# Optimization experiments

Measured on AMD Instinct MI355X. Metric: run time of the kernel, lower is better.

## Reference

```python
import jax, jax.numpy as jnp
import numpy as np

PLOGIT_INIT = 1.5

def setup_inputs() -> dict:
    key = jax.random.key(0)
    B, C, H, W = 32, 256, 64, 64
    x = jax.random.normal(key, (B, C, H, W), dtype=jnp.float32)
    plogit = jnp.full((C,), PLOGIT_INIT, dtype=jnp.float32)  # learned param (post channel-expansion)
    return {"input": x, "plogit": plogit}


def reference(input, plogit):
    B, C = input.shape[0], input.shape[1]
    x = input.reshape(B * C, -1)                       # [B*C, HW]  (to_cw)
    s = jnp.sort(x, axis=-1)                           # per-row full sort
    N = s.shape[1]
    p = jax.nn.sigmoid(plogit)                         # [C]
    # torch: p.view(1,-1).repeat(B,1).view(-1) -> channel-major tiling over batch
    p_full = jnp.tile(p, B)                            # [B*C]
    # torch indexes with int(N * p.data[0] -/+ 0.02): a single scalar column index
    p0 = jax.lax.stop_gradient(p[0])
    i_low = jnp.clip((N * (p0 - 0.02)).astype(jnp.int32), 0, N - 1)
    i_high = jnp.clip((N * (p0 + 0.02)).astype(jnp.int32), 0, N - 1)
    x_low = jax.lax.stop_gradient(jnp.take(s, i_low, axis=1))    # [B*C], detached
    x_high = jax.lax.stop_gradient(jnp.take(s, i_high, axis=1))  # [B*C], detached
    thr = x_low + (x_high - x_low) * p_full            # linear interp, grad flows via p
    thr = thr.reshape(B, C, 1, 1)                      # from_cw
    return jax.nn.relu(input - thr)
```

## Files before the change

kernel.cpp:

```cpp
#include <hip/hip_runtime.h>
#include <math.h>

#define NTHREADS 256
#define NELEM    4096
#define VPT      4
#define NPART    8
#define HSTRIDE  257

__device__ __forceinline__ unsigned f2ord(float f) {
    unsigned u = __float_as_uint(f);
    return (u & 0x80000000u) ? ~u : (u | 0x80000000u);
}
__device__ __forceinline__ float ord2f(unsigned k) {
    unsigned u = (k & 0x80000000u) ? (k ^ 0x80000000u) : ~k;
    return __uint_as_float(u);
}

__device__ __forceinline__ void histo_pass(const unsigned* keys, unsigned* hist,
                                           unsigned known, unsigned pref, int shift, int tid) {
    for (int i = tid; i < NPART * HSTRIDE; i += NTHREADS) hist[i] = 0u;
    __syncthreads();
    unsigned* myh = hist + (tid & (NPART - 1)) * HSTRIDE;
    const uint4* kp = (const uint4*)keys;
    #pragma unroll
    for (int j = 0; j < VPT; ++j) {
        uint4 kk = kp[j * NTHREADS + tid];
        unsigned karr[4] = {kk.x, kk.y, kk.z, kk.w};
        #pragma unroll
        for (int e = 0; e < 4; ++e) {
            unsigned k = karr[e];
            if ((k & known) == pref)
                atomicAdd(&myh[(k >> shift) & 0xFFu], 1u);
        }
    }
    __syncthreads();
}

__device__ __forceinline__ void scan_pick(const unsigned* hist, unsigned* scanbuf,
                                          int tid, unsigned rA, unsigned rB, bool doB,
                                          unsigned* sh) {
    unsigned cnt = 0;
    #pragma unroll
    for (int p = 0; p < NPART; ++p) cnt += hist[p * HSTRIDE + tid];
    scanbuf[tid] = cnt;
    __syncthreads();
    for (int off = 1; off < NTHREADS; off <<= 1) {
        unsigned add = (tid >= off) ? scanbuf[tid - off] : 0u;
        __syncthreads();
        scanbuf[tid] += add;
        __syncthreads();
    }
    unsigned inc = scanbuf[tid];
    unsigned exc = tid ? scanbuf[tid - 1] : 0u;
    if (rA >= exc && rA < inc) { sh[0] = (unsigned)tid; sh[1] = rA - exc; }
    if (doB && rB >= exc && rB < inc) { sh[2] = (unsigned)tid; sh[3] = rB - exc; }
    __syncthreads();
}

__global__ void __launch_bounds__(NTHREADS)
xsrelu_kernel(const float* __restrict__ x, const float* __restrict__ plogit,
              float* __restrict__ out, int C) {
    __shared__ __align__(16) unsigned keys[NELEM];
    __shared__ unsigned hist[NPART * HSTRIDE];
    __shared__ unsigned scanbuf[NTHREADS];
    __shared__ unsigned sh[4];

    const int tid = threadIdx.x;
    const int row = blockIdx.x;
    const float4* xr = (const float4*)(x + (size_t)row * NELEM);

    float4 v[VPT];
    #pragma unroll
    for (int j = 0; j < VPT; ++j) {
        v[j] = xr[j * NTHREADS + tid];
        int base = (j * NTHREADS + tid) * 4;
        keys[base + 0] = f2ord(v[j].x);
        keys[base + 1] = f2ord(v[j].y);
        keys[base + 2] = f2ord(v[j].z);
        keys[base + 3] = f2ord(v[j].w);
    }

    float p0 = 1.0f / (1.0f + expf(-plogit[0]));
    int c = row % C;
    float pc = 1.0f / (1.0f + expf(-plogit[c]));

    int kLow  = (int)((float)NELEM * (p0 - 0.02f));
    int kHigh = (int)((float)NELEM * (p0 + 0.02f));
    kLow  = min(max(kLow, 0),  NELEM - 1);
    kHigh = min(max(kHigh, 0), NELEM - 1);

    __syncthreads();

    unsigned prefA = 0, prefB = 0, known = 0;
    unsigned rA = (unsigned)kLow, rB = (unsigned)kHigh;
    bool diverged = false;

    for (int shift = 24; shift >= 0; shift -= 8) {
        histo_pass(keys, hist, known, prefA, shift, tid);
        scan_pick(hist, scanbuf, tid, rA, rB, !diverged, sh);
        unsigned bA = sh[0], nrA = sh[1];
        if (!diverged) {
            unsigned bB = sh[2], nrB = sh[3];
            prefB = prefA | (bB << shift);
            prefA = prefA | (bA << shift);
            rA = nrA; rB = nrB;
            if (bA != bB) diverged = true;
        } else {
            prefA |= (bA << shift);
            rA = nrA;
            histo_pass(keys, hist, known, prefB, shift, tid);
            scan_pick(hist, scanbuf, tid, rB, rB, false, sh);
            prefB |= (sh[0] << shift);
            rB = sh[1];
        }
        known |= (0xFFu << shift);
    }

    float xlow  = ord2f(prefA);
    float xhigh = ord2f(prefB);
    float thr = xlow + (xhigh - xlow) * pc;

    float4* outr = (float4*)(out + (size_t)row * NELEM);
    #pragma unroll
    for (int j = 0; j < VPT; ++j) {
        float4 o;
        o.x = fmaxf(v[j].x - thr, 0.0f);
        o.y = fmaxf(v[j].y - thr, 0.0f);
        o.z = fmaxf(v[j].z - thr, 0.0f);
        o.w = fmaxf(v[j].w - thr, 0.0f);
        outr[j * NTHREADS + tid] = o;
    }
}

extern "C" void kernel_launch(void* const* d_in, const int* in_sizes, int n_in,
                              void* d_out, int out_size, void* d_ws, size_t ws_size,
                              hipStream_t stream) {
    const float* x      = (const float*)d_in[0];
    const float* plogit = (const float*)d_in[1];
    float* out          = (float*)d_out;
    int C    = in_sizes[1];
    int rows = in_sizes[0] / NELEM;
    xsrelu_kernel<<<rows, NTHREADS, 0, stream>>>(x, plogit, out, C);
}
```

Measured before the change: 267.8 us.

## Replace shared-memory radix select with per-wave register bisection using ballot counts

Each wavefront now processes one row, holding its 4096 keys in registers (64 per lane), and finds the two order statistics by binary search over the 32-bit key space. Each step counts keys at or below the midpoint with ballot and popcount. This removes the shared-memory histograms, atomics, block-level scans and barriers. In exchange it performs up to 64 bisection steps of 64 compares each per row, and raises register pressure.

After: 366.9 us. 37.0% more time.

```diff
diff --git a/kernel.cpp b/kernel.cpp
--- a/kernel.cpp
+++ b/kernel.cpp
@@ -3,9 +3,7 @@
 
 #define NTHREADS 256
 #define NELEM    4096
-#define VPT      4
-#define NPART    8
-#define HSTRIDE  257
+#define EPL      64
 
 __device__ __forceinline__ unsigned f2ord(float f) {
     unsigned u = __float_as_uint(f);
@@ -16,68 +14,44 @@
     return __uint_as_float(u);
 }
 
-__device__ __forceinline__ void histo_pass(const unsigned* keys, unsigned* hist,
-                                           unsigned known, unsigned pref, int shift, int tid) {
-    for (int i = tid; i < NPART * HSTRIDE; i += NTHREADS) hist[i] = 0u;
-    __syncthreads();
-    unsigned* myh = hist + (tid & (NPART - 1)) * HSTRIDE;
-    const uint4* kp = (const uint4*)keys;
+__device__ __forceinline__ unsigned count_leq(const unsigned* k, unsigned t) {
+    unsigned c = 0;
     #pragma unroll
-    for (int j = 0; j < VPT; ++j) {
-        uint4 kk = kp[j * NTHREADS + tid];
-        unsigned karr[4] = {kk.x, kk.y, kk.z, kk.w};
-        #pragma unroll
-        for (int e = 0; e < 4; ++e) {
-            unsigned k = karr[e];
-            if ((k & known) == pref)
-                atomicAdd(&myh[(k >> shift) & 0xFFu], 1u);
-        }
+    for (int j = 0; j < EPL; ++j) {
+        c += (unsigned)__popcll(__ballot(k[j] <= t));
     }
-    __syncthreads();
+    return c;
 }
 
-__device__ __forceinline__ void scan_pick(const unsigned* hist, unsigned* scanbuf,
-                                          int tid, unsigned rA, unsigned rB, bool doB,
-                                          unsigned* sh) {
-    unsigned cnt = 0;
-    #pragma unroll
-    for (int p = 0; p < NPART; ++p) cnt += hist[p * HSTRIDE + tid];
-    scanbuf[tid] = cnt;
-    __syncthreads();
-    for (int off = 1; off < NTHREADS; off <<= 1) {
-        unsigned add = (tid >= off) ? scanbuf[tid - off] : 0u;
-        __syncthreads();
-        scanbuf[tid] += add;
-        __syncthreads();
+__device__ __forceinline__ unsigned bisect(const unsigned* k, unsigned rank) {
+    unsigned lo = 0u, hi = 0xFFFFFFFFu;
+    #pragma unroll 1
+    for (int it = 0; it < 32; ++it) {
+        if (lo >= hi) break;
+        unsigned mid = lo + ((hi - lo) >> 1);
+        if (count_leq(k, mid) >= rank + 1u) hi = mid;
+        else                                lo = mid + 1u;
     }
-    unsigned inc = scanbuf[tid];
-    unsigned exc = tid ? scanbuf[tid - 1] : 0u;
-    if (rA >= exc && rA < inc) { sh[0] = (unsigned)tid; sh[1] = rA - exc; }
-    if (doB && rB >= exc && rB < inc) { sh[2] = (unsigned)tid; sh[3] = rB - exc; }
-    __syncthreads();
+    return lo;
 }
 
 __global__ void __launch_bounds__(NTHREADS)
 xsrelu_kernel(const float* __restrict__ x, const float* __restrict__ plogit,
               float* __restrict__ out, int C) {
-    __shared__ __align__(16) unsigned keys[NELEM];
-    __shared__ unsigned hist[NPART * HSTRIDE];
-    __shared__ unsigned scanbuf[NTHREADS];
-    __shared__ unsigned sh[4];
+    const int wave = threadIdx.x >> 6;
+    const int lane = threadIdx.x & 63;
+    const int row  = blockIdx.x * 4 + wave;
 
-    const int tid = threadIdx.x;
-    const int row = blockIdx.x;
     const float4* xr = (const float4*)(x + (size_t)row * NELEM);
 
-    float4 v[VPT];
+    unsigned k[EPL];
     #pragma unroll
-    for (int j = 0; j < VPT; ++j) {
-        v[j] = xr[j * NTHREADS + tid];
-        int base = (j * NTHREADS + tid) * 4;
-        keys[base + 0] = f2ord(v[j].x);
-        keys[base + 1] = f2ord(v[j].y);
-        keys[base + 2] = f2ord(v[j].z);
-        keys[base + 3] = f2ord(v[j].w);
+    for (int j = 0; j < EPL / 4; ++j) {
+        float4 v = xr[j * 64 + lane];
+        k[4 * j + 0] = f2ord(v.x);
+        k[4 * j + 1] = f2ord(v.y);
+        k[4 * j + 2] = f2ord(v.z);
+        k[4 * j + 3] = f2ord(v.w);
     }
 
     float p0 = 1.0f / (1.0f + expf(-plogit[0]));
@@ -86,49 +60,25 @@
 
     int kLow  = (int)((float)NELEM * (p0 - 0.02f));
     int kHigh = (int)((float)NELEM * (p0 + 0.02f));
-    kLow  = min(max(kLow, 0),  NELEM - 1);
+    kLow  = min(max(kLow,  0), NELEM - 1);
     kHigh = min(max(kHigh, 0), NELEM - 1);
 
-    __syncthreads();
+    unsigned keyLow  = bisect(k, (unsigned)kLow);
+    unsigned keyHigh = bisect(k, (unsigned)kHigh);
 
-    unsigned prefA = 0, prefB = 0, known = 0;
-    unsigned rA = (unsigned)kLow, rB = (unsigned)kHigh;
-    bool diverged = false;
-
-    for (int shift = 24; shift >= 0; shift -= 8) {
-        histo_pass(keys, hist, known, prefA, shift, tid);
-        scan_pick(hist, scanbuf, tid, rA, rB, !diverged, sh);
-        unsigned bA = sh[0], nrA = sh[1];
-        if (!diverged) {
-            unsigned bB = sh[2], nrB = sh[3];
-            prefB = prefA | (bB << shift);
-            prefA = prefA | (bA << shift);
-            rA = nrA; rB = nrB;
-            if (bA != bB) diverged = true;
-        } else {
-            prefA |= (bA << shift);
-            rA = nrA;
-            histo_pass(keys, hist, known, prefB, shift, tid);
-            scan_pick(hist, scanbuf, tid, rB, rB, false, sh);
-            prefB |= (sh[0] << shift);
-            rB = sh[1];
-        }
-        known |= (0xFFu << shift);
-    }
-
-    float xlow  = ord2f(prefA);
-    float xhigh = ord2f(prefB);
+    float xlow  = ord2f(keyLow);
+    float xhigh = ord2f(keyHigh);
     float thr = xlow + (xhigh - xlow) * pc;
 
     float4* outr = (float4*)(out + (size_t)row * NELEM);
     #pragma unroll
-    for (int j = 0; j < VPT; ++j) {
+    for (int j = 0; j < EPL / 4; ++j) {
         float4 o;
-        o.x = fmaxf(v[j].x - thr, 0.0f);
-        o.y = fmaxf(v[j].y - thr, 0.0f);
-        o.z = fmaxf(v[j].z - thr, 0.0f);
-        o.w = fmaxf(v[j].w - thr, 0.0f);
-        outr[j * NTHREADS + tid] = o;
+        o.x = fmaxf(ord2f(k[4 * j + 0]) - thr, 0.0f);
+        o.y = fmaxf(ord2f(k[4 * j + 1]) - thr, 0.0f);
+        o.z = fmaxf(ord2f(k[4 * j + 2]) - thr, 0.0f);
+        o.w = fmaxf(ord2f(k[4 * j + 3]) - thr, 0.0f);
+        outr[j * 64 + lane] = o;
     }
 }
 
@@ -140,5 +90,5 @@
     float* out          = (float*)d_out;
     int C    = in_sizes[1];
     int rows = in_sizes[0] / NELEM;
-    xsrelu_kernel<<<rows, NTHREADS, 0, stream>>>(x, plogit, out, C);
+    xsrelu_kernel<<<rows / 4, NTHREADS, 0, stream>>>(x, plogit, out, C);
 }
```
